# Performance work log

Hardware: AMD Instinct MI355X
Metric: run time of the kernel (lower is better)

## Reference

```python
import jax, jax.numpy as jnp
import numpy as np

B, C, P, T = 16, 128, 512, 32
H = 2
D = C // H  # 64
SCALE = D ** -0.5  # note: original scales by d^-0.5, NOT (d*t)^-0.5


def setup_inputs() -> dict:
    key = jax.random.key(0)
    kx, kw, kb = jax.random.split(key, 3)
    x = jax.random.normal(kx, (B, C, P, T), dtype=jnp.float32)
    # Conv2d(C, 3C, kernel=1) == per-pixel linear: W:[3C, C], b:[3C]
    W = jax.random.normal(kw, (3 * C, C), dtype=jnp.float32) * (C ** -0.5)
    b = jax.random.normal(kb, (3 * C,), dtype=jnp.float32) * 0.01
    return {"x": x, "W": W, "b": b}


def reference(x, W, b):
    # 1x1 conv -> pointwise channel mix
    qkv = jnp.einsum('bcpt,oc->bopt', x, W) + b[None, :, None, None]  # [B,3C,P,T]
    qkv = qkv.reshape(B, 3, H, D, P, T)
    q, k, v = qkv[:, 0], qkv[:, 1], qkv[:, 2]  # each [B,H,D,P,T]
    # flatten (d t) as feature dim, tokens along P
    q = q.transpose(0, 1, 3, 2, 4).reshape(B, H, P, D * T)
    k = k.transpose(0, 1, 3, 2, 4).reshape(B, H, P, D * T)
    v = v.transpose(0, 1, 3, 2, 4).reshape(B, H, P, D * T)
    dots = jnp.einsum('bhpe,bhqe->bhpq', q, k) * SCALE  # [B,H,P,P]
    attn = jax.nn.softmax(dots, axis=-1)
    out = jnp.einsum('bhpq,bhqe->bhpe', attn, v)  # [B,H,P,D*T]
    # b h p (d t) -> b (h d) p t
    out = out.reshape(B, H, P, D, T).transpose(0, 1, 3, 2, 4).reshape(B, C, P, T)
    return out
```

## Files before the change

### kernel.cpp

```cpp
#include <hip/hip_runtime.h>

#define BB 16
#define CC 128
#define PP 512
#define TT 32
#define HH 2
#define DD 64
#define EE 2048
#define NPIX 16384
#define SCALE 0.125f

typedef _Float16 f16_t;
typedef _Float16 f16x8_t __attribute__((ext_vector_type(8)));
typedef _Float16 f16x4_t __attribute__((ext_vector_type(4)));
typedef float    f32x4_t __attribute__((ext_vector_type(4)));

#define AS_GLOBAL __attribute__((address_space(1)))
#define AS_LDS    __attribute__((address_space(3)))

__device__ __forceinline__ void async_ld16(const void* g, void* l) {
    __builtin_amdgcn_global_load_lds((const AS_GLOBAL void*)g,
                                     (AS_LDS void*)l, 16, 0, 0);
}

__device__ __forceinline__ void gemm_lds_bt(const f16_t* __restrict__ A, int lda,
                                            const f16_t* __restrict__ Bt, int ldb,
                                            int K, int m0, int n0,
                                            f16_t* As, f16_t* Bs,
                                            f32x4_t acc[4][4])
{
    const int tid  = threadIdx.x;
    const int lane = tid & 63;
    const int wave = tid >> 6;
    const int wm = wave & 1, wn = wave >> 1;
    const int quad = lane >> 4, l16 = lane & 15;

    const f16_t* gA0 = A  + (size_t)(m0 + lane)      * lda + wave * 8;
    const f16_t* gA1 = A  + (size_t)(m0 + 64 + lane) * lda + wave * 8;
    const f16_t* gB0 = Bt + (size_t)(n0 + lane)      * ldb + wave * 8;
    const f16_t* gB1 = Bt + (size_t)(n0 + 64 + lane) * ldb + wave * 8;
    f16_t* lA0 = As + (size_t)(wave * 128)      * 8;
    f16_t* lA1 = As + (size_t)(wave * 128 + 64) * 8;
    f16_t* lB0 = Bs + (size_t)(wave * 128)      * 8;
    f16_t* lB1 = Bs + (size_t)(wave * 128 + 64) * 8;

    const int ar = wm * 64 + l16;
    const int br = wn * 64 + l16;

    for (int k0 = 0; k0 < K; k0 += 32) {
        if (k0) __syncthreads();
        async_ld16(gA0 + k0, lA0);
        async_ld16(gA1 + k0, lA1);
        async_ld16(gB0 + k0, lB0);
        async_ld16(gB1 + k0, lB1);
        __syncthreads();

        f16x8_t af[4], bf[4];
#pragma unroll
        for (int mi = 0; mi < 4; ++mi)
            af[mi] = *(const f16x8_t*)(As + (size_t)(quad * 128 + ar + mi * 16) * 8);
#pragma unroll
        for (int ni = 0; ni < 4; ++ni)
            bf[ni] = *(const f16x8_t*)(Bs + (size_t)(quad * 128 + br + ni * 16) * 8);
#pragma unroll
        for (int mi = 0; mi < 4; ++mi)
#pragma unroll
            for (int ni = 0; ni < 4; ++ni)
                acc[mi][ni] = __builtin_amdgcn_mfma_f32_16x16x32_f16(
                    af[mi], bf[ni], acc[mi][ni], 0, 0, 0);
    }
}

__global__ __launch_bounds__(256) void wcvt_kernel(const float* __restrict__ W,
                                                   f16_t* __restrict__ Wh)
{
    const int i = (blockIdx.x * 256 + threadIdx.x) * 4;
    const float4 wv = *(const float4*)(W + i);
    f16x4_t t;
    t[0] = (_Float16)wv.x; t[1] = (_Float16)wv.y;
    t[2] = (_Float16)wv.z; t[3] = (_Float16)wv.w;
    *(f16x4_t*)(Wh + i) = t;
}

__global__ __launch_bounds__(256) void proj_kernel(const float* __restrict__ x,
                                                   const f16_t* __restrict__ Wh,
                                                   const float* __restrict__ bias,
                                                   f16_t* __restrict__ q,
                                                   f16_t* __restrict__ k,
                                                   f16_t* __restrict__ v)
{
    __shared__ f16_t xs[CC * 128];
    const int b    = blockIdx.y;
    const int pt   = blockIdx.x;
    const int tid  = threadIdx.x;
    const int lane = tid & 63;
    const int wave = tid >> 6;
    const int wm   = wave & 1, wn = wave >> 1;
    const int quad = lane >> 4, l16 = lane & 15;
    const int pixb = pt * 128;

    const float* xb = x + (size_t)b * CC * NPIX;

#pragma unroll 2
    for (int r = 0; r < 8; ++r) {
        const int u  = r * 4 + wave;
        const int c0 = (u >> 1) * 8;
        const int pl = (u & 1) * 64 + lane;
        const float* g = xb + (size_t)c0 * NPIX + pixb + pl;
        float vv[8];
#pragma unroll
        for (int j = 0; j < 8; ++j) vv[j] = g[(size_t)j * NPIX];
        f16x8_t t;
#pragma unroll
        for (int j = 0; j < 8; ++j) t[j] = (_Float16)vv[j];
        *(f16x8_t*)((char*)xs + pl * 256 + ((c0 * 2) ^ ((pl & 15) << 4))) = t;
    }
    __syncthreads();

    for (int s = 0; s < 3; ++s) {
        f32x4_t acc[4][4];
#pragma unroll
        for (int i = 0; i < 4; ++i)
#pragma unroll
            for (int j = 0; j < 4; ++j) acc[i][j] = (f32x4_t){0.f, 0.f, 0.f, 0.f};

#pragma unroll
        for (int k0 = 0; k0 < CC; k0 += 32) {
            const int kq = k0 + quad * 8;
            f16x8_t xf[4], wf[4];
#pragma unroll
            for (int mi = 0; mi < 4; ++mi) {
                const int pl = wm * 64 + mi * 16 + l16;
                xf[mi] = *(const f16x8_t*)((char*)xs + pl * 256 +
                                           ((kq * 2) ^ ((pl & 15) << 4)));
            }
#pragma unroll
            for (int ni = 0; ni < 4; ++ni) {
                const int o = s * 128 + wn * 64 + ni * 16 + l16;
                wf[ni] = *(const f16x8_t*)(Wh + (size_t)o * CC + kq);
            }
#pragma unroll
            for (int mi = 0; mi < 4; ++mi)
#pragma unroll
                for (int ni = 0; ni < 4; ++ni)
                    acc[mi][ni] = __builtin_amdgcn_mfma_f32_16x16x32_f16(
                        xf[mi], wf[ni], acc[mi][ni], 0, 0, 0);
        }

        f16_t* dst = (s == 0) ? q : (s == 1) ? k : v;
        float bv[4];
#pragma unroll
        for (int ni = 0; ni < 4; ++ni)
            bv[ni] = bias[s * 128 + wn * 64 + ni * 16 + l16];

        const int h = wn;
#pragma unroll
        for (int mi = 0; mi < 4; ++mi) {
            const int pix0 = pixb + wm * 64 + mi * 16 + quad * 4;
            const int p  = pix0 >> 5;
            const int t0 = pix0 & 31;
#pragma unroll
            for (int ni = 0; ni < 4; ++ni) {
                const int d = ni * 16 + l16;
                f16x4_t o4;
#pragma unroll
                for (int r = 0; r < 4; ++r)
                    o4[r] = (_Float16)(acc[mi][ni][r] + bv[ni]);
                *(f16x4_t*)(dst + ((size_t)((b * HH + h) * PP + p)) * EE
                                + d * TT + t0) = o4;
            }
        }
    }
}

__global__ __launch_bounds__(256) void vpose_kernel(const f16_t* __restrict__ v,
                                                    f16_t* __restrict__ vt)
{
    __shared__ unsigned short lds[64][65];
    const int bh   = blockIdx.y;
    const int tile = blockIdx.x;
    const int e0 = (tile & 31) * 64;
    const int p0 = (tile >> 5) * 64;
    const int tid = threadIdx.x;
    const int rw  = tid >> 3;
    const int c8  = (tid & 7) * 8;
    const f16_t* vb  = v  + (size_t)bh * PP * EE;
    f16_t*       vtb = vt + (size_t)bh * EE * PP;
#pragma unroll
    for (int half = 0; half < 2; ++half) {
        const int p = rw + half * 32;
        const f16x8_t t = *(const f16x8_t*)(vb + (size_t)(p0 + p) * EE + e0 + c8);
#pragma unroll
        for (int j = 0; j < 8; ++j)
            lds[p][c8 + j] = __builtin_bit_cast(unsigned short, (_Float16)t[j]);
    }
    __syncthreads();
#pragma unroll
    for (int half = 0; half < 2; ++half) {
        const int e = rw + half * 32;
        f16x8_t t;
#pragma unroll
        for (int j = 0; j < 8; ++j)
            t[j] = __builtin_bit_cast(_Float16, lds[c8 + j][e]);
        *(f16x8_t*)(vtb + (size_t)(e0 + e) * PP + p0 + c8) = t;
    }
}

__global__ __launch_bounds__(256) void qk_kernel(const f16_t* __restrict__ q,
                                                 const f16_t* __restrict__ k,
                                                 float* __restrict__ S)
{
    __shared__ f16_t As[128 * 32];
    __shared__ f16_t Bs[128 * 32];
    const int id = blockIdx.x;
    const int bh = id & 31;
    const int tile = id >> 5;
    const int mt = tile & 3, nt = tile >> 2;
    const int tid  = threadIdx.x;
    const int lane = tid & 63;
    const int wave = tid >> 6;
    const int wm = wave & 1, wn = wave >> 1;
    const int quad = lane >> 4, l16 = lane & 15;

    f32x4_t acc[4][4];
#pragma unroll
    for (int i = 0; i < 4; ++i)
#pragma unroll
        for (int j = 0; j < 4; ++j) acc[i][j] = (f32x4_t){0.f, 0.f, 0.f, 0.f};

    const f16_t* qb = q + (size_t)bh * PP * EE;
    const f16_t* kb = k + (size_t)bh * PP * EE;
    gemm_lds_bt(qb, EE, kb, EE, EE, mt * 128, nt * 128, As, Bs, acc);

    float* Sb = S + (size_t)bh * PP * PP;
#pragma unroll
    for (int mi = 0; mi < 4; ++mi)
#pragma unroll
        for (int r = 0; r < 4; ++r) {
            const int row = mt * 128 + wm * 64 + mi * 16 + quad * 4 + r;
#pragma unroll
            for (int ni = 0; ni < 4; ++ni) {
                const int col = nt * 128 + wn * 64 + ni * 16 + l16;
                Sb[(size_t)row * PP + col] = acc[mi][ni][r] * SCALE;
            }
        }
}

__global__ __launch_bounds__(256) void softmax_kernel(float* __restrict__ S)
{
    const int tid  = threadIdx.x;
    const int wave = tid >> 6;
    const int lane = tid & 63;
    const int row  = blockIdx.x * 4 + wave;
    float* rp = S + (size_t)row * PP;

    const float4 a = *(const float4*)(rp + lane * 8);
    const float4 b = *(const float4*)(rp + lane * 8 + 4);

    float m = fmaxf(fmaxf(fmaxf(a.x, a.y), fmaxf(a.z, a.w)),
                    fmaxf(fmaxf(b.x, b.y), fmaxf(b.z, b.w)));
#pragma unroll
    for (int off = 1; off < 64; off <<= 1) m = fmaxf(m, __shfl_xor(m, off, 64));

    float e[8];
    e[0] = expf(a.x - m); e[1] = expf(a.y - m);
    e[2] = expf(a.z - m); e[3] = expf(a.w - m);
    e[4] = expf(b.x - m); e[5] = expf(b.y - m);
    e[6] = expf(b.z - m); e[7] = expf(b.w - m);

    float sum = e[0] + e[1] + e[2] + e[3] + e[4] + e[5] + e[6] + e[7];
#pragma unroll
    for (int off = 1; off < 64; off <<= 1) sum += __shfl_xor(sum, off, 64);
    const float inv = 1.0f / sum;

    __syncthreads();

    f16_t* prow = (f16_t*)rp;
    f16x8_t o;
#pragma unroll
    for (int j = 0; j < 8; ++j) o[j] = (_Float16)(e[j] * inv);
    *(f16x8_t*)(prow + lane * 8) = o;
}

__global__ __launch_bounds__(256) void pv_kernel(const f16_t* __restrict__ Pm,
                                                 const f16_t* __restrict__ vt,
                                                 float* __restrict__ out)
{
    __shared__ f16_t As[128 * 32];
    __shared__ f16_t Bs[128 * 32];
    const int id = blockIdx.x;
    const int bh = id & 31;
    const int tile = id >> 5;
    const int nt = tile & 3, mt = tile >> 2;
    const int tid  = threadIdx.x;
    const int lane = tid & 63;
    const int wave = tid >> 6;
    const int wm = wave & 1, wn = wave >> 1;
    const int quad = lane >> 4, l16 = lane & 15;

    f32x4_t acc[4][4];
#pragma unroll
    for (int i = 0; i < 4; ++i)
#pragma unroll
        for (int j = 0; j < 4; ++j) acc[i][j] = (f32x4_t){0.f, 0.f, 0.f, 0.f};

    const f16_t* Pb  = Pm + (size_t)bh * PP * 1024;
    const f16_t* vtb = vt + (size_t)bh * EE * PP;
    gemm_lds_bt(vtb, PP, Pb, 1024, PP, mt * 128, nt * 128, As, Bs, acc);

    const int b = bh >> 1, h = bh & 1;
#pragma unroll
    for (int mi = 0; mi < 4; ++mi) {
        const int e0 = mt * 128 + wm * 64 + mi * 16 + quad * 4;
        const int d  = e0 >> 5;
        const int t0 = e0 & 31;
#pragma unroll
        for (int ni = 0; ni < 4; ++ni) {
            const int p = nt * 128 + wn * 64 + ni * 16 + l16;
            *(f32x4_t*)(out + ((size_t)(b * CC + h * DD + d) * PP + p) * TT + t0)
                = acc[mi][ni];
        }
    }
}

extern "C" void kernel_launch(void* const* d_in, const int* in_sizes, int n_in,
                              void* d_out, int out_size, void* d_ws, size_t ws_size,
                              hipStream_t stream)
{
    const float* x    = (const float*)d_in[0];
    const float* W    = (const float*)d_in[1];
    const float* bias = (const float*)d_in[2];
    float* out = (float*)d_out;

    char* ws = (char*)d_ws;
    const size_t MiB = 1024ull * 1024ull;
    f16_t* q  = (f16_t*)(ws);
    f16_t* k  = (f16_t*)(ws + 64 * MiB);
    f16_t* v  = (f16_t*)(ws + 128 * MiB);
    f16_t* vt = (f16_t*)(ws + 192 * MiB);
    float* S  = (float*)(ws + 256 * MiB);
    f16_t* Wh = (f16_t*)(ws + 256 * MiB);

    wcvt_kernel<<<dim3(48), dim3(256), 0, stream>>>(W, Wh);
    proj_kernel<<<dim3(128, 16), dim3(256), 0, stream>>>(x, Wh, bias, q, k, v);
    vpose_kernel<<<dim3(256, 32), dim3(256), 0, stream>>>(v, vt);
    qk_kernel<<<dim3(512), dim3(256), 0, stream>>>(q, k, S);
    softmax_kernel<<<dim3(4096), dim3(256), 0, stream>>>(S);
    pv_kernel<<<dim3(2048), dim3(256), 0, stream>>>((const f16_t*)S, vt, out);
}
```

Baseline: 503.3 us.

## Stage projection weights in LDS and coalesce QKV output stores through LDS

The projection kernel now asynchronously loads each 128-row weight slice into an LDS buffer with global_load_lds before the MFMA loop, instead of reading weight fragments straight from global memory. The same LDS buffer is then reused to stage the biased fp16 output tile with an XOR swizzle, and the tile is written back as fully contiguous 16-byte-per-lane rows. The goal is to cut scattered global weight reads and strided 8-byte output stores. The cost is extra LDS traffic and several more __syncthreads per slice.

After: 498.5 us. About the same (-0.9%).

```diff
diff --git a/kernel.cpp b/kernel.cpp
--- a/kernel.cpp
+++ b/kernel.cpp
@@ -90,6 +90,7 @@
                                                    f16_t* __restrict__ v)
 {
     __shared__ f16_t xs[CC * 128];
+    __shared__ f16_t wbuf[16 * 128 * 8];
     const int b    = blockIdx.y;
     const int pt   = blockIdx.x;
     const int tid  = threadIdx.x;
@@ -115,9 +116,18 @@
         for (int j = 0; j < 8; ++j) t[j] = (_Float16)vv[j];
         *(f16x8_t*)((char*)xs + pl * 256 + ((c0 * 2) ^ ((pl & 15) << 4))) = t;
     }
-    __syncthreads();
 
     for (int s = 0; s < 3; ++s) {
+#pragma unroll
+        for (int i = 0; i < 8; ++i) {
+            const int idx = wave * 8 + i;
+            const int ch  = idx >> 1;
+            const int oh  = (idx & 1) * 64;
+            async_ld16(Wh + (size_t)(s * 128 + oh + lane) * CC + ch * 8,
+                       wbuf + ((size_t)ch * 128 + oh) * 8);
+        }
+        __syncthreads();
+
         f32x4_t acc[4][4];
 #pragma unroll
         for (int i = 0; i < 4; ++i)
@@ -126,7 +136,8 @@
 
 #pragma unroll
         for (int k0 = 0; k0 < CC; k0 += 32) {
-            const int kq = k0 + quad * 8;
+            const int kq  = k0 + quad * 8;
+            const int chq = (k0 >> 3) + quad;
             f16x8_t xf[4], wf[4];
 #pragma unroll
             for (int mi = 0; mi < 4; ++mi) {
@@ -136,8 +147,8 @@
             }
 #pragma unroll
             for (int ni = 0; ni < 4; ++ni) {
-                const int o = s * 128 + wn * 64 + ni * 16 + l16;
-                wf[ni] = *(const f16x8_t*)(Wh + (size_t)o * CC + kq);
+                const int ol = wn * 64 + ni * 16 + l16;
+                wf[ni] = *(const f16x8_t*)(wbuf + ((size_t)chq * 128 + ol) * 8);
             }
 #pragma unroll
             for (int mi = 0; mi < 4; ++mi)
@@ -147,18 +158,19 @@
                         xf[mi], wf[ni], acc[mi][ni], 0, 0, 0);
         }
 
-        f16_t* dst = (s == 0) ? q : (s == 1) ? k : v;
         float bv[4];
 #pragma unroll
         for (int ni = 0; ni < 4; ++ni)
             bv[ni] = bias[s * 128 + wn * 64 + ni * 16 + l16];
 
-        const int h = wn;
+        __syncthreads();
+
+        f16_t* obuf = wbuf;
 #pragma unroll
         for (int mi = 0; mi < 4; ++mi) {
-            const int pix0 = pixb + wm * 64 + mi * 16 + quad * 4;
-            const int p  = pix0 >> 5;
-            const int t0 = pix0 & 31;
+            const int pixl = wm * 64 + mi * 16 + quad * 4;
+            const int p  = pixl >> 5;
+            const int t0 = pixl & 31;
 #pragma unroll
             for (int ni = 0; ni < 4; ++ni) {
                 const int d = ni * 16 + l16;
@@ -166,10 +178,27 @@
 #pragma unroll
                 for (int r = 0; r < 4; ++r)
                     o4[r] = (_Float16)(acc[mi][ni][r] + bv[ni]);
-                *(f16x4_t*)(dst + ((size_t)((b * HH + h) * PP + p)) * EE
-                                + d * TT + t0) = o4;
+                const int ebyte = (((wn * 4 + p) * 64 + d) * 32 + t0) * 2;
+                *(f16x4_t*)((char*)obuf + (ebyte ^ ((d & 3) << 4))) = o4;
             }
         }
+        __syncthreads();
+
+        f16_t* dst = (s == 0) ? q : (s == 1) ? k : v;
+        const int hr  = tid >> 5;
+        const int l32 = tid & 31;
+        f16_t* drow = dst + ((size_t)((b * HH + (hr >> 2)) * PP)
+                             + pt * 4 + (hr & 3)) * EE;
+#pragma unroll
+        for (int j = 0; j < 8; ++j) {
+            const int d  = j * 8 + (l32 >> 2);
+            const int tb = (l32 & 3) * 16;
+            const f16x8_t t8 = *(const f16x8_t*)((char*)obuf
+                                + (size_t)(hr * 64 + d) * 64
+                                + (tb ^ ((d & 3) << 4)));
+            *(f16x8_t*)((char*)drow + j * 512 + l32 * 16) = t8;
+        }
+        __syncthreads();
     }
 }
 
```
